# Performance work log

Measured on AMD Instinct MI355X. Metric: run time of the kernel, lower is better.

The kernel has to match this reference:

```python
import jax, jax.numpy as jnp
import numpy as np

BITS = 8
EPS = 1e-5
NUM_HEADS = 16


def quantize_weight(w, eps=EPS):
    # per-tensor abs-mean scale, ternary weights in {-1, 0, 1}
    scale = jnp.maximum(jnp.mean(jnp.abs(w)), eps)
    qw = jnp.clip(jnp.round(w / scale), -1.0, 1.0)
    return qw, scale


def bitlinear158_inference(x, qw, scale, bias=None, bits=BITS, eps=EPS):
    # per-token abs-max activation quantization to [-Q, Q-1]
    q = float(2 ** (bits - 1))
    gamma = jnp.maximum(jnp.max(jnp.abs(x), axis=-1, keepdims=True), eps)
    qx = jnp.clip(jnp.round(x * (q / gamma)), -q, q - 1.0)
    out = jnp.einsum('...i,oi->...o', qx, qw)
    out = out * (scale * gamma / q)
    if bias is not None:
        out = out + bias
    return out


def setup_inputs() -> dict:
    rng = jax.random.key(0)
    ks = jax.random.split(rng, 7)
    B, L, E = 4, 2048, 1024
    return {
        'query': jax.random.normal(ks[0], (B, L, E), jnp.float32),
        'key': jax.random.normal(ks[1], (B, L, E), jnp.float32),
        'value': jax.random.normal(ks[2], (B, L, E), jnp.float32),
        'in_proj_weight': jax.random.normal(ks[3], (3 * E, E), jnp.float32) * 0.02,
        'in_proj_bias': jax.random.normal(ks[4], (3 * E,), jnp.float32) * 0.02,
        'out_proj_weight': jax.random.normal(ks[5], (E, E), jnp.float32) * 0.02,
        'out_proj_bias': jax.random.normal(ks[6], (E,), jnp.float32) * 0.02,
    }


def reference(query, key, value, in_proj_weight, in_proj_bias, out_proj_weight, out_proj_bias):
    B, Lq, E = query.shape
    Lk = key.shape[1]
    H = NUM_HEADS
    D = E // H

    # quantize weights as done at __init__ time
    qw, kw, vw = jnp.split(in_proj_weight, 3, axis=0)  # each [E, E]
    qb, kb, vb = jnp.split(in_proj_bias, 3, axis=0)
    q_qw, q_s = quantize_weight(qw)
    k_qw, k_s = quantize_weight(kw)
    v_qw, v_s = quantize_weight(vw)
    o_qw, o_s = quantize_weight(out_proj_weight)

    # quantized projections [B, L, E]
    q = bitlinear158_inference(query, q_qw, q_s, qb)
    k = bitlinear158_inference(key, k_qw, k_s, kb)
    v = bitlinear158_inference(value, v_qw, v_s, vb)

    # [B, H, L, D]
    q = q.reshape(B, Lq, H, D).transpose(0, 2, 1, 3)
    k = k.reshape(B, Lk, H, D).transpose(0, 2, 1, 3)
    v = v.reshape(B, Lk, H, D).transpose(0, 2, 1, 3)

    scores = jnp.einsum('bhqd,bhkd->bhqk', q, k) / jnp.sqrt(jnp.asarray(D, q.dtype))
    attn = jax.nn.softmax(scores, axis=-1)
    ctx = jnp.einsum('bhqk,bhkd->bhqd', attn, v)  # [B, H, Lq, D]
    ctx = ctx.transpose(0, 2, 1, 3).reshape(B, Lq, E)

    out = bitlinear158_inference(ctx, o_qw, o_s, out_proj_bias)
    return out
```

## Files before the change

### kernel.cpp

```cpp
#include <hip/hip_runtime.h>
#include <cstdint>
#include <cstddef>

#define BB 4
#define LL 2048
#define EE 1024
#define HH 16
#define DD 64
#define TT (BB*LL)
#define EPSF 1e-5f

typedef _Float16 half8 __attribute__((ext_vector_type(8)));
typedef _Float16 half4v __attribute__((ext_vector_type(4)));
typedef float floatx4 __attribute__((ext_vector_type(4)));
typedef float floatx16 __attribute__((ext_vector_type(16)));

__device__ __forceinline__ void gl_lds16(const void* g, void* l) {
    __builtin_amdgcn_global_load_lds(
        (const __attribute__((address_space(1))) void*)g,
        (__attribute__((address_space(3))) void*)l, 16, 0, 0);
}

__global__ void k_absum(const float* __restrict__ in_proj,
                        const float* __restrict__ out_proj,
                        double* __restrict__ sums) {
    const int which = blockIdx.y;
    const float* src = (which < 3) ? (in_proj + (size_t)which * EE * EE) : out_proj;
    double loc = 0.0;
    const int n = EE * EE;
    for (int i = blockIdx.x * blockDim.x + threadIdx.x; i < n; i += gridDim.x * blockDim.x)
        loc += (double)fabsf(src[i]);
    #pragma unroll
    for (int off = 32; off > 0; off >>= 1) loc += __shfl_down(loc, off, 64);
    __shared__ double red[4];
    const int lane = threadIdx.x & 63, wv = threadIdx.x >> 6;
    if (lane == 0) red[wv] = loc;
    __syncthreads();
    if (threadIdx.x == 0) {
        double tot = red[0] + red[1] + red[2] + red[3];
        atomicAdd(&sums[which], tot);
    }
}

__global__ void k_quantw(const float* __restrict__ in_proj,
                         const float* __restrict__ out_proj,
                         const double* __restrict__ sums,
                         float* __restrict__ scaleF,
                         _Float16* __restrict__ qwh) {
    const int idx = blockIdx.x * blockDim.x + threadIdx.x;
    if (idx < 4) scaleF[idx] = fmaxf((float)(sums[idx] * (1.0 / (EE * EE))), EPSF);
    const int which = idx >> 20;
    const float s = fmaxf((float)(sums[which] * (1.0 / (EE * EE))), EPSF);
    const float w = (which < 3) ? in_proj[idx] : out_proj[idx - 3 * EE * EE];
    float q = rintf(w / s);
    q = fminf(fmaxf(q, -1.f), 1.f);
    qwh[idx] = (_Float16)q;
}

__global__ __launch_bounds__(256) void k_gammaq(const float* __restrict__ x,
                                                float* __restrict__ g,
                                                _Float16* __restrict__ qx) {
    const int wv = threadIdx.x >> 6, lane = threadIdx.x & 63;
    const int tok = blockIdx.x * 4 + wv;
    const float* xp = x + (size_t)tok * EE;
    float4 v[4];
    #pragma unroll
    for (int i = 0; i < 4; i++) v[i] = *(const float4*)(xp + (lane + 64 * i) * 4);
    float m = 0.f;
    #pragma unroll
    for (int i = 0; i < 4; i++)
        m = fmaxf(m, fmaxf(fmaxf(fabsf(v[i].x), fabsf(v[i].y)),
                           fmaxf(fabsf(v[i].z), fabsf(v[i].w))));
    #pragma unroll
    for (int off = 1; off < 64; off <<= 1) m = fmaxf(m, __shfl_xor(m, off, 64));
    const float gg = fmaxf(m, EPSF);
    const float rg = 128.f / gg;
    _Float16* qp = qx + (size_t)tok * EE;
    #pragma unroll
    for (int i = 0; i < 4; i++) {
        half4v h;
        h[0] = (_Float16)fminf(fmaxf(rintf(v[i].x * rg), -128.f), 127.f);
        h[1] = (_Float16)fminf(fmaxf(rintf(v[i].y * rg), -128.f), 127.f);
        h[2] = (_Float16)fminf(fmaxf(rintf(v[i].z * rg), -128.f), 127.f);
        h[3] = (_Float16)fminf(fmaxf(rintf(v[i].w * rg), -128.f), 127.f);
        *(half4v*)(qp + (lane + 64 * i) * 4) = h;
    }
    if (lane == 0) g[tok] = gg;
}

__global__ __launch_bounds__(256) void k_bitmm(
    const _Float16* __restrict__ qx, const float* __restrict__ gam,
    const _Float16* __restrict__ qw, const float* __restrict__ scaleF, int widx,
    const float* __restrict__ bias, float* __restrict__ outF,
    _Float16* __restrict__ outH, int mode, float pre) {
    __shared__ __align__(16) _Float16 As[128][64];
    __shared__ __align__(16) _Float16 Bs[128][64];
    const int tid = threadIdx.x;
    const int wv = tid >> 6, lane = tid & 63;
    const int quad = lane >> 4, l16 = lane & 15;
    const int wm = wv & 1, wn = wv >> 1;
    const int t0 = blockIdx.x * 128, o0 = blockIdx.y * 128;
    const int srow = lane >> 3, schunk = lane & 7;

    floatx4 acc[4][4];
    #pragma unroll
    for (int i = 0; i < 4; i++)
        #pragma unroll
        for (int j = 0; j < 4; j++) acc[i][j] = (floatx4){0.f, 0.f, 0.f, 0.f};

    for (int k0 = 0; k0 < EE; k0 += 64) {
        __syncthreads();
        #pragma unroll
        for (int p = 0; p < 4; p++) {
            const int r2 = wv * 4 + p;
            const int c = schunk ^ srow ^ (r2 & 7);
            const int row = r2 * 8 + srow;
            gl_lds16(qx + (size_t)(t0 + row) * EE + k0 + c * 8, &As[r2 * 8][0]);
            gl_lds16(qw + (size_t)(o0 + row) * EE + k0 + c * 8, &Bs[r2 * 8][0]);
        }
        __syncthreads();
        #pragma unroll
        for (int kk = 0; kk < 2; kk++) {
            half8 af[4], bf[4];
            #pragma unroll
            for (int s4 = 0; s4 < 4; s4++) {
                const int mA = (l16 & 7) ^ ((s4 * 2 + (l16 >> 3)) & 7);
                af[s4] = *(const half8*)&As[wm * 64 + s4 * 16 + l16][((kk * 4 + quad) ^ mA) * 8];
                bf[s4] = *(const half8*)&Bs[wn * 64 + s4 * 16 + l16][((kk * 4 + quad) ^ mA) * 8];
            }
            #pragma unroll
            for (int sm = 0; sm < 4; sm++)
                #pragma unroll
                for (int sn = 0; sn < 4; sn++)
                    acc[sm][sn] = __builtin_amdgcn_mfma_f32_16x16x32_f16(
                        af[sm], bf[sn], acc[sm][sn], 0, 0, 0);
        }
    }

    const float s = scaleF[widx];
    #pragma unroll
    for (int sm = 0; sm < 4; sm++) {
        #pragma unroll
        for (int r = 0; r < 4; r++) {
            const int t = t0 + wm * 64 + sm * 16 + quad * 4 + r;
            const float mr = s * gam[t] * 0.0078125f;
            const int b_ = t >> 11, l_ = t & (LL - 1);
            #pragma unroll
            for (int sn = 0; sn < 4; sn++) {
                const int o = o0 + wn * 64 + sn * 16 + l16;
                const float val = acc[sm][sn][r] * mr + bias[o];
                if (mode == 0) {
                    outF[(size_t)t * EE + o] = val;
                } else if (mode == 1) {
                    const int h_ = o >> 6, d_ = o & 63;
                    outH[((size_t)(b_ * HH + h_) * LL + l_) * DD + d_] = (_Float16)(val * pre);
                } else {
                    const int h_ = o >> 6, d_ = o & 63;
                    outH[((size_t)(b_ * HH + h_) * DD + d_) * LL + l_] = (_Float16)val;
                }
            }
        }
    }
}

__global__ __launch_bounds__(256, 4) void k_attn3(const _Float16* __restrict__ Q,
                                                  const _Float16* __restrict__ K,
                                                  const _Float16* __restrict__ Vt,
                                                  float* __restrict__ ctx) {
    __shared__ __align__(16) _Float16 Ksh[64][64];
    __shared__ __align__(16) _Float16 Vtsh[64][64];
    __shared__ __align__(16) _Float16 Pq[4][32][64];
    const int tid = threadIdx.x;
    const int wv = tid >> 6, lane = tid & 63;
    const int l32 = lane & 31, h2 = lane >> 5;
    const int bh = blockIdx.y, b_ = bh >> 4, h_ = bh & 15;
    const int q0 = blockIdx.x * 128 + wv * 32;
    const int srow = lane >> 3, schunk = lane & 7;

    const _Float16* Qb = Q + (size_t)bh * LL * DD;
    const _Float16* Kb = K + (size_t)bh * LL * DD;
    const _Float16* Vtb = Vt + (size_t)bh * DD * LL;

    half8 qf[4];
    #pragma unroll
    for (int ds = 0; ds < 4; ds++)
        qf[ds] = *(const half8*)(Qb + (size_t)(q0 + l32) * DD + ds * 16 + h2 * 8);

    floatx16 acc[2];
    #pragma unroll
    for (int r = 0; r < 16; r++) { acc[0][r] = 0.f; acc[1][r] = 0.f; }
    float lsum = 0.f;

    const int maskP = (l32 & 7) ^ ((l32 >> 3) & 7);

    for (int kt = 0; kt < LL; kt += 64) {
        __syncthreads();
        #pragma unroll
        for (int u = 0; u < 2; u++) {
            const int g = wv * 2 + u;
            const int c = schunk ^ srow ^ (g & 7);
            const int row = g * 8 + srow;
            gl_lds16(Kb + (size_t)(kt + row) * DD + c * 8, &Ksh[g * 8][0]);
            gl_lds16(Vtb + (size_t)row * LL + kt + c * 8, &Vtsh[g * 8][0]);
        }
        __syncthreads();

        #pragma unroll
        for (int ks = 0; ks < 2; ks++) {
            const int rowK = ks * 32 + l32;
            const int maskK = (l32 & 7) ^ ((rowK >> 3) & 7);
            floatx16 s;
            #pragma unroll
            for (int r = 0; r < 16; r++) s[r] = 0.f;
            #pragma unroll
            for (int ds = 0; ds < 4; ds++) {
                const half8 kf = *(const half8*)&Ksh[rowK][((2 * ds + h2) ^ maskK) * 8];
                s = __builtin_amdgcn_mfma_f32_32x32x16_f16(kf, qf[ds], s, 0, 0, 0);
            }
            #pragma unroll
            for (int c4 = 0; c4 < 4; c4++) {
                const float p0 = __builtin_amdgcn_exp2f(s[c4 * 4 + 0]);
                const float p1 = __builtin_amdgcn_exp2f(s[c4 * 4 + 1]);
                const float p2 = __builtin_amdgcn_exp2f(s[c4 * 4 + 2]);
                const float p3 = __builtin_amdgcn_exp2f(s[c4 * 4 + 3]);
                lsum += (p0 + p1) + (p2 + p3);
                half4v ph;
                ph[0] = (_Float16)p0; ph[1] = (_Float16)p1;
                ph[2] = (_Float16)p2; ph[3] = (_Float16)p3;
                const int keyc = ks * 4 + c4;
                *(half4v*)&Pq[wv][l32][((keyc ^ maskP) * 8) + h2 * 4] = ph;
            }
        }

        half8 pa[4];
        #pragma unroll
        for (int ks2 = 0; ks2 < 4; ks2++) {
            const int keyc = ks2 * 2 + h2;
            pa[ks2] = *(const half8*)&Pq[wv][l32][((keyc ^ maskP) * 8)];
        }
        #pragma unroll
        for (int sd = 0; sd < 2; sd++) {
            const int rowV = sd * 32 + l32;
            const int maskV = (l32 & 7) ^ ((rowV >> 3) & 7);
            #pragma unroll
            for (int ks2 = 0; ks2 < 4; ks2++) {
                const half8 vf = *(const half8*)&Vtsh[rowV][((2 * ks2 + h2) ^ maskV) * 8];
                acc[sd] = __builtin_amdgcn_mfma_f32_32x32x16_f16(pa[ks2], vf, acc[sd], 0, 0, 0);
            }
        }
    }

    lsum += __shfl_xor(lsum, 32, 64);
    const float invl = 1.f / lsum;
    #pragma unroll
    for (int r = 0; r < 16; r++) {
        const int qrow = 8 * (r >> 2) + 4 * h2 + (r & 3);
        const float iv = __shfl(invl, qrow, 64);
        float* cp = ctx + ((size_t)b_ * LL + q0 + qrow) * EE + h_ * DD + l32;
        cp[0]  = acc[0][r] * iv;
        cp[32] = acc[1][r] * iv;
    }
}

extern "C" void kernel_launch(void* const* d_in, const int* in_sizes, int n_in,
                              void* d_out, int out_size, void* d_ws, size_t ws_size,
                              hipStream_t stream) {
    const float* query      = (const float*)d_in[0];
    const float* key        = (const float*)d_in[1];
    const float* value      = (const float*)d_in[2];
    const float* in_proj_w  = (const float*)d_in[3];
    const float* in_proj_b  = (const float*)d_in[4];
    const float* out_proj_w = (const float*)d_in[5];
    const float* out_proj_b = (const float*)d_in[6];
    float* out = (float*)d_out;

    char* ws = (char*)d_ws;
    double*   sums   = (double*)ws;
    float*    scaleF = (float*)(ws + 32);
    float*    gbuf   = (float*)(ws + 256);
    _Float16* qwh    = (_Float16*)(ws + (size_t)262144);
    _Float16* qxh    = (_Float16*)(ws + (size_t)16 * 1024 * 1024);
    _Float16* Qh     = (_Float16*)(ws + (size_t)64 * 1024 * 1024);
    _Float16* Kh     = Qh + (size_t)TT * EE;
    _Float16* Vth    = Kh + (size_t)TT * EE;
    float*    ctx    = out;

    const float QPRE = 0.18033688011112042f;

    hipMemsetAsync(sums, 0, 32, stream);
    k_absum<<<dim3(64, 4), 256, 0, stream>>>(in_proj_w, out_proj_w, sums);
    k_quantw<<<(4 * EE * EE) / 256, 256, 0, stream>>>(in_proj_w, out_proj_w, sums, scaleF, qwh);
    k_gammaq<<<TT / 4, 256, 0, stream>>>(query, gbuf + 0 * TT, qxh + 0 * (size_t)TT * EE);
    k_gammaq<<<TT / 4, 256, 0, stream>>>(key,   gbuf + 1 * TT, qxh + 1 * (size_t)TT * EE);
    k_gammaq<<<TT / 4, 256, 0, stream>>>(value, gbuf + 2 * TT, qxh + 2 * (size_t)TT * EE);

    dim3 gg(TT / 128, EE / 128);
    k_bitmm<<<gg, 256, 0, stream>>>(qxh + 0 * (size_t)TT * EE, gbuf + 0 * TT,
                                    qwh + 0 * (size_t)EE * EE, scaleF, 0,
                                    in_proj_b + 0,    nullptr, Qh, 1, QPRE);
    k_bitmm<<<gg, 256, 0, stream>>>(qxh + 1 * (size_t)TT * EE, gbuf + 1 * TT,
                                    qwh + 1 * (size_t)EE * EE, scaleF, 1,
                                    in_proj_b + 1024, nullptr, Kh, 1, 1.0f);
    k_bitmm<<<gg, 256, 0, stream>>>(qxh + 2 * (size_t)TT * EE, gbuf + 2 * TT,
                                    qwh + 2 * (size_t)EE * EE, scaleF, 2,
                                    in_proj_b + 2048, nullptr, Vth, 2, 1.0f);

    k_attn3<<<dim3(LL / 128, BB * HH), 256, 0, stream>>>(Qh, Kh, Vth, ctx);

    k_gammaq<<<TT / 4, 256, 0, stream>>>(ctx, gbuf + 3 * TT, qxh + 0 * (size_t)TT * EE);
    k_bitmm<<<gg, 256, 0, stream>>>(qxh + 0 * (size_t)TT * EE, gbuf + 3 * TT,
                                    qwh + 3 * (size_t)EE * EE, scaleF, 3,
                                    out_proj_b, out, nullptr, 0, 1.0f);
}
```

Before: 414.7 us.

## Switch bit-linear GEMMs to int8 MFMA and restructure attention kernel

Quantized activations and ternary weights are now stored as int8 and multiplied with the i32 16x16x64 int8 MFMA using 128-wide K tiles, which halves the operand bytes and doubles MFMA throughput per instruction. The V projection epilogue stages its tile in LDS so the transposed V write is coalesced. The attention kernel handles 64 query rows per wave and keeps the softmax probabilities in registers, repacked with lane shuffles, instead of going through LDS. The new code raises register pressure in attention and drops the explicit occupancy hint.

Result: faster. 368.6 us (-11.1%).

```diff
diff --git a/kernel.cpp b/kernel.cpp
--- a/kernel.cpp
+++ b/kernel.cpp
@@ -14,11 +14,19 @@
 typedef _Float16 half4v __attribute__((ext_vector_type(4)));
 typedef float floatx4 __attribute__((ext_vector_type(4)));
 typedef float floatx16 __attribute__((ext_vector_type(16)));
+typedef int intx4 __attribute__((ext_vector_type(4)));
+typedef unsigned int uintx4 __attribute__((ext_vector_type(4)));
 
 __device__ __forceinline__ void gl_lds16(const void* g, void* l) {
     __builtin_amdgcn_global_load_lds(
         (const __attribute__((address_space(1))) void*)g,
         (__attribute__((address_space(3))) void*)l, 16, 0, 0);
+}
+
+__device__ __forceinline__ uint32_t pk2(float a, float b) {
+    union { _Float16 h[2]; uint32_t u; } x;
+    x.h[0] = (_Float16)a; x.h[1] = (_Float16)b;
+    return x.u;
 }
 
 __global__ void k_absum(const float* __restrict__ in_proj,
@@ -46,7 +54,7 @@
                          const float* __restrict__ out_proj,
                          const double* __restrict__ sums,
                          float* __restrict__ scaleF,
-                         _Float16* __restrict__ qwh) {
+                         int8_t* __restrict__ qw) {
     const int idx = blockIdx.x * blockDim.x + threadIdx.x;
     if (idx < 4) scaleF[idx] = fmaxf((float)(sums[idx] * (1.0 / (EE * EE))), EPSF);
     const int which = idx >> 20;
@@ -54,12 +62,12 @@
     const float w = (which < 3) ? in_proj[idx] : out_proj[idx - 3 * EE * EE];
     float q = rintf(w / s);
     q = fminf(fmaxf(q, -1.f), 1.f);
-    qwh[idx] = (_Float16)q;
+    qw[idx] = (int8_t)q;
 }
 
 __global__ __launch_bounds__(256) void k_gammaq(const float* __restrict__ x,
                                                 float* __restrict__ g,
-                                                _Float16* __restrict__ qx) {
+                                                int8_t* __restrict__ qx) {
     const int wv = threadIdx.x >> 6, lane = threadIdx.x & 63;
     const int tok = blockIdx.x * 4 + wv;
     const float* xp = x + (size_t)tok * EE;
@@ -75,69 +83,99 @@
     for (int off = 1; off < 64; off <<= 1) m = fmaxf(m, __shfl_xor(m, off, 64));
     const float gg = fmaxf(m, EPSF);
     const float rg = 128.f / gg;
-    _Float16* qp = qx + (size_t)tok * EE;
+    int8_t* qp = qx + (size_t)tok * EE;
     #pragma unroll
     for (int i = 0; i < 4; i++) {
-        half4v h;
-        h[0] = (_Float16)fminf(fmaxf(rintf(v[i].x * rg), -128.f), 127.f);
-        h[1] = (_Float16)fminf(fmaxf(rintf(v[i].y * rg), -128.f), 127.f);
-        h[2] = (_Float16)fminf(fmaxf(rintf(v[i].z * rg), -128.f), 127.f);
-        h[3] = (_Float16)fminf(fmaxf(rintf(v[i].w * rg), -128.f), 127.f);
-        *(half4v*)(qp + (lane + 64 * i) * 4) = h;
+        char4 c;
+        c.x = (int8_t)(int)fminf(fmaxf(rintf(v[i].x * rg), -128.f), 127.f);
+        c.y = (int8_t)(int)fminf(fmaxf(rintf(v[i].y * rg), -128.f), 127.f);
+        c.z = (int8_t)(int)fminf(fmaxf(rintf(v[i].z * rg), -128.f), 127.f);
+        c.w = (int8_t)(int)fminf(fmaxf(rintf(v[i].w * rg), -128.f), 127.f);
+        *(char4*)(qp + (lane + 64 * i) * 4) = c;
     }
     if (lane == 0) g[tok] = gg;
 }
 
 __global__ __launch_bounds__(256) void k_bitmm(
-    const _Float16* __restrict__ qx, const float* __restrict__ gam,
-    const _Float16* __restrict__ qw, const float* __restrict__ scaleF, int widx,
+    const int8_t* __restrict__ qx, const float* __restrict__ gam,
+    const int8_t* __restrict__ qw, const float* __restrict__ scaleF, int widx,
     const float* __restrict__ bias, float* __restrict__ outF,
     _Float16* __restrict__ outH, int mode, float pre) {
-    __shared__ __align__(16) _Float16 As[128][64];
-    __shared__ __align__(16) _Float16 Bs[128][64];
+    __shared__ __align__(16) int8_t smem[36864];
+    int8_t (*As)[128] = (int8_t(*)[128])smem;
+    int8_t (*Bs)[128] = (int8_t(*)[128])(smem + 16384);
+    _Float16 (*Vt)[136] = (_Float16(*)[136])smem;
     const int tid = threadIdx.x;
     const int wv = tid >> 6, lane = tid & 63;
     const int quad = lane >> 4, l16 = lane & 15;
     const int wm = wv & 1, wn = wv >> 1;
     const int t0 = blockIdx.x * 128, o0 = blockIdx.y * 128;
     const int srow = lane >> 3, schunk = lane & 7;
-
-    floatx4 acc[4][4];
+    const int cc = schunk ^ srow;
+
+    intx4 acc[4][4];
     #pragma unroll
     for (int i = 0; i < 4; i++)
         #pragma unroll
-        for (int j = 0; j < 4; j++) acc[i][j] = (floatx4){0.f, 0.f, 0.f, 0.f};
-
-    for (int k0 = 0; k0 < EE; k0 += 64) {
+        for (int j = 0; j < 4; j++) acc[i][j] = (intx4){0, 0, 0, 0};
+
+    for (int k0 = 0; k0 < EE; k0 += 128) {
         __syncthreads();
         #pragma unroll
         for (int p = 0; p < 4; p++) {
-            const int r2 = wv * 4 + p;
-            const int c = schunk ^ srow ^ (r2 & 7);
-            const int row = r2 * 8 + srow;
-            gl_lds16(qx + (size_t)(t0 + row) * EE + k0 + c * 8, &As[r2 * 8][0]);
-            gl_lds16(qw + (size_t)(o0 + row) * EE + k0 + c * 8, &Bs[r2 * 8][0]);
+            const int row = wv * 32 + p * 8 + srow;
+            gl_lds16(qx + (size_t)(t0 + row) * EE + k0 + cc * 16, &As[wv * 32 + p * 8][0]);
+            gl_lds16(qw + (size_t)(o0 + row) * EE + k0 + cc * 16, &Bs[wv * 32 + p * 8][0]);
         }
         __syncthreads();
         #pragma unroll
         for (int kk = 0; kk < 2; kk++) {
-            half8 af[4], bf[4];
+            intx4 af[4], bf[4];
             #pragma unroll
             for (int s4 = 0; s4 < 4; s4++) {
-                const int mA = (l16 & 7) ^ ((s4 * 2 + (l16 >> 3)) & 7);
-                af[s4] = *(const half8*)&As[wm * 64 + s4 * 16 + l16][((kk * 4 + quad) ^ mA) * 8];
-                bf[s4] = *(const half8*)&Bs[wn * 64 + s4 * 16 + l16][((kk * 4 + quad) ^ mA) * 8];
+                const int ph = ((kk * 4 + quad) ^ (l16 & 7)) * 16;
+                af[s4] = *(const intx4*)&As[wm * 64 + s4 * 16 + l16][ph];
+                bf[s4] = *(const intx4*)&Bs[wn * 64 + s4 * 16 + l16][ph];
             }
             #pragma unroll
             for (int sm = 0; sm < 4; sm++)
                 #pragma unroll
                 for (int sn = 0; sn < 4; sn++)
-                    acc[sm][sn] = __builtin_amdgcn_mfma_f32_16x16x32_f16(
+                    acc[sm][sn] = __builtin_amdgcn_mfma_i32_16x16x64_i8(
                         af[sm], bf[sn], acc[sm][sn], 0, 0, 0);
         }
     }
 
     const float s = scaleF[widx];
+    if (mode == 2) {
+        __syncthreads();
+        #pragma unroll
+        for (int sm = 0; sm < 4; sm++) {
+            const int tl = wm * 64 + sm * 16 + quad * 4;
+            float mr[4];
+            #pragma unroll
+            for (int r = 0; r < 4; r++) mr[r] = s * gam[t0 + tl + r] * 0.0078125f;
+            #pragma unroll
+            for (int sn = 0; sn < 4; sn++) {
+                const int ol = wn * 64 + sn * 16 + l16;
+                const float b = bias[o0 + ol];
+                half4v hv;
+                #pragma unroll
+                for (int r = 0; r < 4; r++)
+                    hv[r] = (_Float16)((float)acc[sm][sn][r] * mr[r] + b);
+                *(half4v*)&Vt[ol][tl] = hv;
+            }
+        }
+        __syncthreads();
+        const int ol2 = tid >> 1, tc0 = (tid & 1) * 64;
+        const int og = o0 + ol2, hh = og >> 6, dd = og & 63;
+        const int bb = t0 >> 11, l0 = t0 & (LL - 1);
+        _Float16* dst = outH + ((size_t)(bb * HH + hh) * DD + dd) * LL + l0 + tc0;
+        #pragma unroll
+        for (int i = 0; i < 8; i++)
+            *(half8*)(dst + i * 8) = *(const half8*)&Vt[ol2][tc0 + i * 8];
+        return;
+    }
     #pragma unroll
     for (int sm = 0; sm < 4; sm++) {
         #pragma unroll
@@ -148,118 +186,135 @@
             #pragma unroll
             for (int sn = 0; sn < 4; sn++) {
                 const int o = o0 + wn * 64 + sn * 16 + l16;
-                const float val = acc[sm][sn][r] * mr + bias[o];
+                const float val = (float)acc[sm][sn][r] * mr + bias[o];
                 if (mode == 0) {
                     outF[(size_t)t * EE + o] = val;
-                } else if (mode == 1) {
+                } else {
                     const int h_ = o >> 6, d_ = o & 63;
                     outH[((size_t)(b_ * HH + h_) * LL + l_) * DD + d_] = (_Float16)(val * pre);
-                } else {
-                    const int h_ = o >> 6, d_ = o & 63;
-                    outH[((size_t)(b_ * HH + h_) * DD + d_) * LL + l_] = (_Float16)val;
                 }
             }
         }
     }
 }
 
-__global__ __launch_bounds__(256, 4) void k_attn3(const _Float16* __restrict__ Q,
-                                                  const _Float16* __restrict__ K,
-                                                  const _Float16* __restrict__ Vt,
-                                                  float* __restrict__ ctx) {
+__global__ __launch_bounds__(256) void k_attn4(const _Float16* __restrict__ Q,
+                                               const _Float16* __restrict__ K,
+                                               const _Float16* __restrict__ Vt,
+                                               float* __restrict__ ctx) {
     __shared__ __align__(16) _Float16 Ksh[64][64];
     __shared__ __align__(16) _Float16 Vtsh[64][64];
-    __shared__ __align__(16) _Float16 Pq[4][32][64];
     const int tid = threadIdx.x;
     const int wv = tid >> 6, lane = tid & 63;
     const int l32 = lane & 31, h2 = lane >> 5;
     const int bh = blockIdx.y, b_ = bh >> 4, h_ = bh & 15;
-    const int q0 = blockIdx.x * 128 + wv * 32;
+    const int q0 = blockIdx.x * 256 + wv * 64;
     const int srow = lane >> 3, schunk = lane & 7;
+    const int cc = schunk ^ srow;
 
     const _Float16* Qb = Q + (size_t)bh * LL * DD;
     const _Float16* Kb = K + (size_t)bh * LL * DD;
     const _Float16* Vtb = Vt + (size_t)bh * DD * LL;
 
-    half8 qf[4];
-    #pragma unroll
-    for (int ds = 0; ds < 4; ds++)
-        qf[ds] = *(const half8*)(Qb + (size_t)(q0 + l32) * DD + ds * 16 + h2 * 8);
-
-    floatx16 acc[2];
-    #pragma unroll
-    for (int r = 0; r < 16; r++) { acc[0][r] = 0.f; acc[1][r] = 0.f; }
-    float lsum = 0.f;
-
-    const int maskP = (l32 & 7) ^ ((l32 >> 3) & 7);
+    half8 qf[2][4];
+    #pragma unroll
+    for (int qh = 0; qh < 2; qh++)
+        #pragma unroll
+        for (int ds = 0; ds < 4; ds++)
+            qf[qh][ds] = *(const half8*)(Qb + (size_t)(q0 + qh * 32 + l32) * DD + ds * 16 + h2 * 8);
+
+    floatx16 acc[2][2];
+    #pragma unroll
+    for (int r = 0; r < 16; r++) {
+        acc[0][0][r] = 0.f; acc[0][1][r] = 0.f; acc[1][0][r] = 0.f; acc[1][1][r] = 0.f;
+    }
+    float lsum[2] = {0.f, 0.f};
 
     for (int kt = 0; kt < LL; kt += 64) {
         __syncthreads();
         #pragma unroll
         for (int u = 0; u < 2; u++) {
-            const int g = wv * 2 + u;
-            const int c = schunk ^ srow ^ (g & 7);
-            const int row = g * 8 + srow;
-            gl_lds16(Kb + (size_t)(kt + row) * DD + c * 8, &Ksh[g * 8][0]);
-            gl_lds16(Vtb + (size_t)row * LL + kt + c * 8, &Vtsh[g * 8][0]);
-        }
-        __syncthreads();
-
+            const int row = wv * 16 + u * 8 + srow;
+            gl_lds16(Kb + (size_t)(kt + row) * DD + cc * 8, &Ksh[wv * 16 + u * 8][0]);
+            gl_lds16(Vtb + (size_t)row * LL + kt + cc * 8, &Vtsh[wv * 16 + u * 8][0]);
+        }
+        __syncthreads();
+
+        half8 pa[4][2];
         #pragma unroll
         for (int ks = 0; ks < 2; ks++) {
             const int rowK = ks * 32 + l32;
-            const int maskK = (l32 & 7) ^ ((rowK >> 3) & 7);
-            floatx16 s;
-            #pragma unroll
-            for (int r = 0; r < 16; r++) s[r] = 0.f;
-            #pragma unroll
-            for (int ds = 0; ds < 4; ds++) {
-                const half8 kf = *(const half8*)&Ksh[rowK][((2 * ds + h2) ^ maskK) * 8];
-                s = __builtin_amdgcn_mfma_f32_32x32x16_f16(kf, qf[ds], s, 0, 0, 0);
-            }
-            #pragma unroll
-            for (int c4 = 0; c4 < 4; c4++) {
-                const float p0 = __builtin_amdgcn_exp2f(s[c4 * 4 + 0]);
-                const float p1 = __builtin_amdgcn_exp2f(s[c4 * 4 + 1]);
-                const float p2 = __builtin_amdgcn_exp2f(s[c4 * 4 + 2]);
-                const float p3 = __builtin_amdgcn_exp2f(s[c4 * 4 + 3]);
-                lsum += (p0 + p1) + (p2 + p3);
-                half4v ph;
-                ph[0] = (_Float16)p0; ph[1] = (_Float16)p1;
-                ph[2] = (_Float16)p2; ph[3] = (_Float16)p3;
-                const int keyc = ks * 4 + c4;
-                *(half4v*)&Pq[wv][l32][((keyc ^ maskP) * 8) + h2 * 4] = ph;
-            }
-        }
-
-        half8 pa[4];
-        #pragma unroll
-        for (int ks2 = 0; ks2 < 4; ks2++) {
-            const int keyc = ks2 * 2 + h2;
-            pa[ks2] = *(const half8*)&Pq[wv][l32][((keyc ^ maskP) * 8)];
-        }
-        #pragma unroll
-        for (int sd = 0; sd < 2; sd++) {
-            const int rowV = sd * 32 + l32;
-            const int maskV = (l32 & 7) ^ ((rowV >> 3) & 7);
-            #pragma unroll
-            for (int ks2 = 0; ks2 < 4; ks2++) {
-                const half8 vf = *(const half8*)&Vtsh[rowV][((2 * ks2 + h2) ^ maskV) * 8];
-                acc[sd] = __builtin_amdgcn_mfma_f32_32x32x16_f16(pa[ks2], vf, acc[sd], 0, 0, 0);
-            }
-        }
-    }
-
-    lsum += __shfl_xor(lsum, 32, 64);
-    const float invl = 1.f / lsum;
-    #pragma unroll
-    for (int r = 0; r < 16; r++) {
-        const int qrow = 8 * (r >> 2) + 4 * h2 + (r & 3);
-        const float iv = __shfl(invl, qrow, 64);
-        float* cp = ctx + ((size_t)b_ * LL + q0 + qrow) * EE + h_ * DD + l32;
-        cp[0]  = acc[0][r] * iv;
-        cp[32] = acc[1][r] * iv;
-    }
+            const int mK = l32 & 7;
+            half8 kf[4];
+            #pragma unroll
+            for (int ds = 0; ds < 4; ds++)
+                kf[ds] = *(const half8*)&Ksh[rowK][((2 * ds + h2) ^ mK) * 8];
+            #pragma unroll
+            for (int qh = 0; qh < 2; qh++) {
+                floatx16 sc;
+                #pragma unroll
+                for (int r = 0; r < 16; r++) sc[r] = 0.f;
+                #pragma unroll
+                for (int ds = 0; ds < 4; ds++)
+                    sc = __builtin_amdgcn_mfma_f32_32x32x16_f16(kf[ds], qf[qh][ds], sc, 0, 0, 0);
+                float p[16];
+                #pragma unroll
+                for (int r = 0; r < 16; r++) p[r] = __builtin_amdgcn_exp2f(sc[r]);
+                #pragma unroll
+                for (int r = 0; r < 16; r++) lsum[qh] += p[r];
+                uint32_t u_[4][2], o_[4][2];
+                #pragma unroll
+                for (int c4 = 0; c4 < 4; c4++) {
+                    u_[c4][0] = pk2(p[4 * c4 + 0], p[4 * c4 + 1]);
+                    u_[c4][1] = pk2(p[4 * c4 + 2], p[4 * c4 + 3]);
+                    o_[c4][0] = __shfl_xor(u_[c4][0], 32, 64);
+                    o_[c4][1] = __shfl_xor(u_[c4][1], 32, 64);
+                }
+                #pragma unroll
+                for (int mm = 0; mm < 2; mm++) {
+                    const uint32_t ua = h2 ? u_[2 * mm + 1][0] : u_[2 * mm][0];
+                    const uint32_t ub = h2 ? u_[2 * mm + 1][1] : u_[2 * mm][1];
+                    const uint32_t oa = h2 ? o_[2 * mm + 1][0] : o_[2 * mm][0];
+                    const uint32_t ob = h2 ? o_[2 * mm + 1][1] : o_[2 * mm][1];
+                    uintx4 w;
+                    w[0] = h2 ? oa : ua;  w[1] = h2 ? ob : ub;
+                    w[2] = h2 ? ua : oa;  w[3] = h2 ? ub : ob;
+                    union { uintx4 u; half8 h; } cv; cv.u = w;
+                    pa[ks * 2 + mm][qh] = cv.h;
+                }
+            }
+        }
+
+        #pragma unroll
+        for (int kb = 0; kb < 4; kb++) {
+            #pragma unroll
+            for (int sd = 0; sd < 2; sd++) {
+                const int rowV = sd * 32 + l32;
+                const half8 vf = *(const half8*)&Vtsh[rowV][((2 * kb + h2) ^ (l32 & 7)) * 8];
+                #pragma unroll
+                for (int qh = 0; qh < 2; qh++)
+                    acc[qh][sd] = __builtin_amdgcn_mfma_f32_32x32x16_f16(
+                        pa[kb][qh], vf, acc[qh][sd], 0, 0, 0);
+            }
+        }
+    }
+
+    float invl[2];
+    #pragma unroll
+    for (int qh = 0; qh < 2; qh++) {
+        lsum[qh] += __shfl_xor(lsum[qh], 32, 64);
+        invl[qh] = 1.f / lsum[qh];
+    }
+    #pragma unroll
+    for (int qh = 0; qh < 2; qh++)
+        #pragma unroll
+        for (int r = 0; r < 16; r++) {
+            const int qrow = (r & 3) + 8 * (r >> 2) + 4 * h2;
+            const float iv = __shfl(invl[qh], qrow, 64);
+            float* cp = ctx + ((size_t)b_ * LL + q0 + qh * 32 + qrow) * EE + h_ * DD + l32;
+            cp[0]  = acc[qh][0][r] * iv;
+            cp[32] = acc[qh][1][r] * iv;
+        }
 }
 
 extern "C" void kernel_launch(void* const* d_in, const int* in_sizes, int n_in,
@@ -278,9 +333,9 @@
     double*   sums   = (double*)ws;
     float*    scaleF = (float*)(ws + 32);
     float*    gbuf   = (float*)(ws + 256);
-    _Float16* qwh    = (_Float16*)(ws + (size_t)262144);
-    _Float16* qxh    = (_Float16*)(ws + (size_t)16 * 1024 * 1024);
-    _Float16* Qh     = (_Float16*)(ws + (size_t)64 * 1024 * 1024);
+    int8_t*   qw8    = (int8_t*)(ws + (size_t)1  * 1024 * 1024);
+    int8_t*   qx8    = (int8_t*)(ws + (size_t)8  * 1024 * 1024);
+    _Float16* Qh     = (_Float16*)(ws + (size_t)40 * 1024 * 1024);
     _Float16* Kh     = Qh + (size_t)TT * EE;
     _Float16* Vth    = Kh + (size_t)TT * EE;
     float*    ctx    = out;
@@ -289,26 +344,26 @@
 
     hipMemsetAsync(sums, 0, 32, stream);
     k_absum<<<dim3(64, 4), 256, 0, stream>>>(in_proj_w, out_proj_w, sums);
-    k_quantw<<<(4 * EE * EE) / 256, 256, 0, stream>>>(in_proj_w, out_proj_w, sums, scaleF, qwh);
-    k_gammaq<<<TT / 4, 256, 0, stream>>>(query, gbuf + 0 * TT, qxh + 0 * (size_t)TT * EE);
-    k_gammaq<<<TT / 4, 256, 0, stream>>>(key,   gbuf + 1 * TT, qxh + 1 * (size_t)TT * EE);
-    k_gammaq<<<TT / 4, 256, 0, stream>>>(value, gbuf + 2 * TT, qxh + 2 * (size_t)TT * EE);
+    k_quantw<<<(4 * EE * EE) / 256, 256, 0, stream>>>(in_proj_w, out_proj_w, sums, scaleF, qw8);
+    k_gammaq<<<TT / 4, 256, 0, stream>>>(query, gbuf + 0 * TT, qx8 + 0 * (size_t)TT * EE);
+    k_gammaq<<<TT / 4, 256, 0, stream>>>(key,   gbuf + 1 * TT, qx8 + 1 * (size_t)TT * EE);
+    k_gammaq<<<TT / 4, 256, 0, stream>>>(value, gbuf + 2 * TT, qx8 + 2 * (size_t)TT * EE);
 
     dim3 gg(TT / 128, EE / 128);
-    k_bitmm<<<gg, 256, 0, stream>>>(qxh + 0 * (size_t)TT * EE, gbuf + 0 * TT,
-                                    qwh + 0 * (size_t)EE * EE, scaleF, 0,
+    k_bitmm<<<gg, 256, 0, stream>>>(qx8 + 0 * (size_t)TT * EE, gbuf + 0 * TT,
+                                    qw8 + 0 * (size_t)EE * EE, scaleF, 0,
                                     in_proj_b + 0,    nullptr, Qh, 1, QPRE);
-    k_bitmm<<<gg, 256, 0, stream>>>(qxh + 1 * (size_t)TT * EE, gbuf + 1 * TT,
-                                    qwh + 1 * (size_t)EE * EE, scaleF, 1,
+    k_bitmm<<<gg, 256, 0, stream>>>(qx8 + 1 * (size_t)TT * EE, gbuf + 1 * TT,
+                                    qw8 + 1 * (size_t)EE * EE, scaleF, 1,
                                     in_proj_b + 1024, nullptr, Kh, 1, 1.0f);
-    k_bitmm<<<gg, 256, 0, stream>>>(qxh + 2 * (size_t)TT * EE, gbuf + 2 * TT,
-                                    qwh + 2 * (size_t)EE * EE, scaleF, 2,
+    k_bitmm<<<gg, 256, 0, stream>>>(qx8 + 2 * (size_t)TT * EE, gbuf + 2 * TT,
+                                    qw8 + 2 * (size_t)EE * EE, scaleF, 2,
                                     in_proj_b + 2048, nullptr, Vth, 2, 1.0f);
 
-    k_attn3<<<dim3(LL / 128, BB * HH), 256, 0, stream>>>(Qh, Kh, Vth, ctx);
-
-    k_gammaq<<<TT / 4, 256, 0, stream>>>(ctx, gbuf + 3 * TT, qxh + 0 * (size_t)TT * EE);
-    k_bitmm<<<gg, 256, 0, stream>>>(qxh + 0 * (size_t)TT * EE, gbuf + 3 * TT,
-                                    qwh + 3 * (size_t)EE * EE, scaleF, 3,
+    k_attn4<<<dim3(LL / 256, BB * HH), 256, 0, stream>>>(Qh, Kh, Vth, ctx);
+
+    k_gammaq<<<TT / 4, 256, 0, stream>>>(ctx, gbuf + 3 * TT, qx8 + 3 * (size_t)TT * EE);
+    k_bitmm<<<gg, 256, 0, stream>>>(qx8 + 3 * (size_t)TT * EE, gbuf + 3 * TT,
+                                    qw8 + 3 * (size_t)EE * EE, scaleF, 3,
                                     out_proj_b, out, nullptr, 0, 1.0f);
 }
```
